# Kernel optimization log

Measured on AMD Instinct MI355X. Metric: run time of the kernel, lower is better.

## Reference

```python
import jax, jax.numpy as jnp
import numpy as np

N = 500_000
E = 16_000_000


def setup_inputs() -> dict:
    key = jax.random.key(0)
    k1, k2, k3, k4, k5 = jax.random.split(key, 5)
    x = jax.random.uniform(k1, (N, 11), dtype=jnp.float32)
    edge_index = jax.random.randint(k2, (2, E), 0, N, dtype=jnp.int32)
    edge_weight = jax.random.uniform(k3, (E,), dtype=jnp.float32)
    W1 = jax.random.normal(k4, (11, 16), dtype=jnp.float32) * 0.3
    b1 = jnp.zeros((16,), jnp.float32)
    W2 = jax.random.normal(k5, (16, 2), dtype=jnp.float32) * 0.3
    b2 = jnp.zeros((2,), jnp.float32)
    return {"x": x, "edge_index": edge_index, "edge_weight": edge_weight,
            "W1": W1, "b1": b1, "W2": W2, "b2": b2}


def gcn_norm(edge_index, edge_weight, n):
    # GCNConv(normalize=True, add_self_loops=True): A_hat = D^-1/2 (A + I) D^-1/2
    self_idx = jnp.arange(n, dtype=edge_index.dtype)
    row = jnp.concatenate([edge_index[0], self_idx])  # source
    col = jnp.concatenate([edge_index[1], self_idx])  # target
    w = jnp.concatenate([edge_weight, jnp.ones((n,), edge_weight.dtype)])
    deg = jax.ops.segment_sum(w, col, num_segments=n)
    dinv = jnp.where(deg > 0, jax.lax.rsqrt(deg), 0.0)
    norm = dinv[row] * w * dinv[col]
    return row, col, norm


def gcn_conv(x, row, col, norm, W, b, n):
    h = x @ W                                   # [N, F_out]
    msg = norm[:, None] * h[row]                # gather + scale, [E+N, F_out]
    out = jax.ops.segment_sum(msg, col, num_segments=n)  # scatter-add
    return out + b


def reference(x, edge_index, edge_weight, W1, b1, W2, b2):
    n = x.shape[0]
    row, col, norm = gcn_norm(edge_index, edge_weight, n)
    h = jax.nn.relu(gcn_conv(x, row, col, norm, W1, b1, n))
    # dropout is identity in eval / deterministic reference
    h = gcn_conv(h, row, col, norm, W2, b2, n)
    return jax.nn.log_softmax(h, axis=1)
```

## Files before the change

kernel.cpp:

```cpp
#include <hip/hip_runtime.h>
#include <math.h>


typedef unsigned long long u64;
typedef unsigned int u32;
typedef unsigned short u16;
typedef _Float16 f16;
typedef __attribute__((ext_vector_type(4))) _Float16 f16x4;

#define BKT    512
#define NBMAX  1024
#define NBLK   512
#define CHUNK  4096


__global__ __launch_bounds__(256) void k_count(const int* __restrict__ col,
                                               u32* __restrict__ hist_g,
                                               int NB, int E, int CH) {
    __shared__ u32 cnt[NBMAX];
    for (int b = threadIdx.x; b < NB; b += 256) cnt[b] = 0;
    __syncthreads();
    int blk = blockIdx.x;
    int s = blk * CH, e = min(s + CH, E);
    for (int i = s + threadIdx.x; i < e; i += 256) {
        int c = __builtin_nontemporal_load(col + i);
        atomicAdd(&cnt[c >> 9], 1u);
    }
    __syncthreads();
    for (int b = threadIdx.x; b < NB; b += 256)
        hist_g[(size_t)blk * NB + b] = cnt[b];
}

__global__ __launch_bounds__(256) void k_colsum(const u32* __restrict__ hist_g,
                                                u32* __restrict__ colsum, int NB) {
    int k = blockIdx.x * 256 + threadIdx.x;
    if (k >= NB) return;
    u32 s = 0;
    for (int j = 0; j < NBLK; j++) s += hist_g[(size_t)j * NB + k];
    colsum[k] = s;
}

__global__ __launch_bounds__(256) void k_scan_sums32(u32* __restrict__ bsum, int nb) {
    __shared__ u32 s[256];
    __shared__ u32 carry;
    int t = threadIdx.x;
    if (t == 0) carry = 0;
    __syncthreads();
    int chunks = (nb + 255) / 256;
    for (int ch = 0; ch < chunks; ch++) {
        int i = ch * 256 + t;
        u32 v = (i < nb) ? bsum[i] : 0;
        s[t] = v;
        __syncthreads();
        for (int off = 1; off < 256; off <<= 1) {
            u32 u = (t >= off) ? s[t - off] : 0;
            __syncthreads();
            s[t] += u;
            __syncthreads();
        }
        u32 incl = s[t];
        u32 my_carry = carry;
        if (i < nb) bsum[i] = incl - v + my_carry;
        __syncthreads();
        if (t == 0) carry = my_carry + s[255];
        __syncthreads();
    }
}

__global__ __launch_bounds__(256) void k_basefill(const u32* __restrict__ hist_g,
                                                  const u32* __restrict__ keybase,
                                                  u32* __restrict__ base_g, int NB) {
    int k = blockIdx.x * 256 + threadIdx.x;
    if (k >= NB) return;
    u32 run = keybase[k];
    for (int j = 0; j < NBLK; j++) {
        base_g[(size_t)j * NB + k] = run;
        run += hist_g[(size_t)j * NB + k];
    }
}


__global__ __launch_bounds__(512) void k_scatter(const int* __restrict__ row,
                                                 const int* __restrict__ col,
                                                 const float* __restrict__ w,
                                                 const u32* __restrict__ base_g,
                                                 u64* __restrict__ edge_g,
                                                 int NB, int E, int CH) {
    __shared__ u64 stage[CHUNK];
    __shared__ u16 skey[CHUNK];
    __shared__ u32 cursor[NBMAX];
    __shared__ u32 ccnt[NBMAX];
    __shared__ u32 cbase[NBMAX];
    __shared__ u32 sscan[512];
    int t = threadIdx.x;
    int blk = blockIdx.x;
    for (int b = t; b < NB; b += 512) cursor[b] = base_g[(size_t)blk * NB + b];
    int s = blk * CH, e = min(s + CH, E);
    for (int c0 = s; c0 < e; c0 += CHUNK) {
        int cend = min(c0 + CHUNK, e);
        for (int b = t; b < NB; b += 512) ccnt[b] = 0;
        __syncthreads();
        u64 rec[8]; u32 rnk[8]; int key[8];
#pragma unroll
        for (int q = 0; q < 8; q++) {
            int i = c0 + q * 512 + t;
            if (i < cend) {
                int c  = __builtin_nontemporal_load(col + i);
                int r  = __builtin_nontemporal_load(row + i);
                float wv = __builtin_nontemporal_load(w + i);
                int k = c >> 9;
                rec[q] = ((u64)__float_as_uint(wv) << 32)
                       | ((u64)(u32)(c & 511) << 19) | (u64)(u32)r;
                key[q] = k;
                rnk[q] = atomicAdd(&ccnt[k], 1u);
            } else key[q] = -1;
        }
        __syncthreads();
        u32 a0 = (2 * t     < NB) ? ccnt[2 * t]     : 0;
        u32 a1 = (2 * t + 1 < NB) ? ccnt[2 * t + 1] : 0;
        sscan[t] = a0 + a1;
        __syncthreads();
        for (int d = 1; d < 512; d <<= 1) {
            u32 v = (t >= d) ? sscan[t - d] : 0;
            __syncthreads();
            sscan[t] += v;
            __syncthreads();
        }
        u32 bse = (t > 0) ? sscan[t - 1] : 0;
        if (2 * t     < NB) cbase[2 * t]     = bse;
        if (2 * t + 1 < NB) cbase[2 * t + 1] = bse + a0;
        __syncthreads();
#pragma unroll
        for (int q = 0; q < 8; q++) {
            if (key[q] >= 0) {
                u32 slot = cbase[key[q]] + rnk[q];
                stage[slot] = rec[q];
                skey[slot] = (u16)key[q];
            }
        }
        __syncthreads();
        int tot = cend - c0;
        for (int j = t; j < tot; j += 512) {
            int k = skey[j];
            edge_g[cursor[k] + (u32)j - cbase[k]] = stage[j];
        }
        __syncthreads();
        for (int b = t; b < NB; b += 512) cursor[b] += ccnt[b];
        __syncthreads();
    }
}


__global__ __launch_bounds__(512) void k_csrsort(const u64* __restrict__ edge_g,
                                                 const u32* __restrict__ kb,
                                                 u64* __restrict__ edge2_g,
                                                 u32* __restrict__ runstart,
                                                 float* __restrict__ dinv_g,
                                                 int NB, int n, int E) {
    __shared__ u64 stage[CHUNK];
    __shared__ u16 skey[CHUNK];
    __shared__ u32 cnt[BKT];
    __shared__ float sdeg[BKT];
    __shared__ u32 cur[BKT];
    __shared__ u32 ccnt[BKT];
    __shared__ u32 cbase[BKT];
    int t = threadIdx.x;
    int b = blockIdx.x;
    int node0 = b << 9;
    int s = (int)kb[b];
    int e = (b + 1 < NB) ? (int)kb[b + 1] : E;
    cnt[t] = 0;
    sdeg[t] = 1.0f;
    __syncthreads();
    for (int i = s + t; i < e; i += 512) {
        u64 rec = __builtin_nontemporal_load(edge_g + i);
        int cl = (int)(((u32)rec >> 19) & 511u);
        atomicAdd(&cnt[cl], 1u);
        atomicAdd(&sdeg[cl], __uint_as_float((u32)(rec >> 32)));
    }
    __syncthreads();
    ccnt[t] = cnt[t];
    __syncthreads();
    for (int d = 1; d < 512; d <<= 1) {
        u32 v = (t >= d) ? ccnt[t - d] : 0;
        __syncthreads();
        ccnt[t] += v;
        __syncthreads();
    }
    u32 mystart = (u32)s + ccnt[t] - cnt[t];
    cur[t] = mystart;
    runstart[node0 + t] = mystart;
    if (t == 511) runstart[node0 + 512] = (u32)e;
    if (node0 + t < n) dinv_g[node0 + t] = rsqrtf(sdeg[t]);
    __syncthreads();
    for (int c0 = s; c0 < e; c0 += CHUNK) {
        int cend = min(c0 + CHUNK, e);
        ccnt[t] = 0;
        __syncthreads();
        u64 rec[8]; u32 rnk[8]; int key[8];
#pragma unroll
        for (int q = 0; q < 8; q++) {
            int i = c0 + q * 512 + t;
            if (i < cend) {
                u64 r = __builtin_nontemporal_load(edge_g + i);
                int cl = (int)(((u32)r >> 19) & 511u);
                rec[q] = r;
                key[q] = cl;
                rnk[q] = atomicAdd(&ccnt[cl], 1u);
            } else key[q] = -1;
        }
        __syncthreads();
        cbase[t] = ccnt[t];
        __syncthreads();
        for (int d = 1; d < 512; d <<= 1) {
            u32 v = (t >= d) ? cbase[t - d] : 0;
            __syncthreads();
            cbase[t] += v;
            __syncthreads();
        }
        u32 myexc = cbase[t] - ccnt[t];
        __syncthreads();
        cbase[t] = myexc;
        __syncthreads();
#pragma unroll
        for (int q = 0; q < 8; q++) {
            if (key[q] >= 0) {
                u32 slot = cbase[key[q]] + rnk[q];
                stage[slot] = rec[q];
                skey[slot] = (u16)key[q];
            }
        }
        __syncthreads();
        int tot = cend - c0;
        for (int j = t; j < tot; j += 512) {
            int k = skey[j];
            edge2_g[cur[k] + (u32)j - cbase[k]] = stage[j];
        }
        __syncthreads();
        cur[t] += ccnt[t];
        __syncthreads();
    }
}


__global__ __launch_bounds__(256) void k_prep(const float* __restrict__ x,
                                              const float* __restrict__ dinv_g,
                                              f16* __restrict__ xs0,
                                              f16* __restrict__ xs1,
                                              f16* __restrict__ xs2, int n) {
    int node = blockIdx.x * 256 + threadIdx.x;
    if (node >= n) return;
    float dv = dinv_g[node];
    const float* xp = x + (size_t)node * 11;
    f16x4 a, bq, c;
#pragma unroll
    for (int k = 0; k < 4; k++) a[k]  = (f16)(dv * xp[k]);
#pragma unroll
    for (int k = 0; k < 4; k++) bq[k] = (f16)(dv * xp[4 + k]);
    c[0] = (f16)(dv * xp[8]);
    c[1] = (f16)(dv * xp[9]);
    c[2] = (f16)(dv * xp[10]);
    c[3] = (f16)0.f;
    *(f16x4*)(xs0 + ((size_t)node << 2)) = a;
    *(f16x4*)(xs1 + ((size_t)node << 2)) = bq;
    *(f16x4*)(xs2 + ((size_t)node << 2)) = c;
}


__global__ __launch_bounds__(256) void k_pass(const u64* __restrict__ edge2_g,
                                              const u32* __restrict__ runstart,
                                              const f16* __restrict__ xsp,
                                              float4* __restrict__ aggp, int n) {
    int node = blockIdx.x * 256 + threadIdx.x;
    if (node >= n) return;
    f16x4 selfv = *(const f16x4*)(xsp + ((size_t)node << 2));
    float a0 = (float)selfv[0], a1 = (float)selfv[1];
    float a2 = (float)selfv[2], a3 = (float)selfv[3];
    int p = (int)runstart[node], pe = (int)runstart[node + 1];
    for (; p + 3 < pe; p += 4) {
        u64 r0 = __builtin_nontemporal_load(edge2_g + p);
        u64 r1 = __builtin_nontemporal_load(edge2_g + p + 1);
        u64 r2 = __builtin_nontemporal_load(edge2_g + p + 2);
        u64 r3 = __builtin_nontemporal_load(edge2_g + p + 3);
        f16x4 g0 = *(const f16x4*)(xsp + ((size_t)((u32)r0 & 0x7FFFFu) << 2));
        f16x4 g1 = *(const f16x4*)(xsp + ((size_t)((u32)r1 & 0x7FFFFu) << 2));
        f16x4 g2 = *(const f16x4*)(xsp + ((size_t)((u32)r2 & 0x7FFFFu) << 2));
        f16x4 g3 = *(const f16x4*)(xsp + ((size_t)((u32)r3 & 0x7FFFFu) << 2));
        float w0 = __uint_as_float((u32)(r0 >> 32));
        float w1 = __uint_as_float((u32)(r1 >> 32));
        float w2 = __uint_as_float((u32)(r2 >> 32));
        float w3 = __uint_as_float((u32)(r3 >> 32));
        a0 += w0 * (float)g0[0] + w1 * (float)g1[0] + w2 * (float)g2[0] + w3 * (float)g3[0];
        a1 += w0 * (float)g0[1] + w1 * (float)g1[1] + w2 * (float)g2[1] + w3 * (float)g3[1];
        a2 += w0 * (float)g0[2] + w1 * (float)g1[2] + w2 * (float)g2[2] + w3 * (float)g3[2];
        a3 += w0 * (float)g0[3] + w1 * (float)g1[3] + w2 * (float)g2[3] + w3 * (float)g3[3];
    }
    for (; p < pe; p++) {
        u64 r0 = edge2_g[p];
        f16x4 g0 = *(const f16x4*)(xsp + ((size_t)((u32)r0 & 0x7FFFFu) << 2));
        float w0 = __uint_as_float((u32)(r0 >> 32));
        a0 += w0 * (float)g0[0];
        a1 += w0 * (float)g0[1];
        a2 += w0 * (float)g0[2];
        a3 += w0 * (float)g0[3];
    }
    float4 ov; ov.x = a0; ov.y = a1; ov.z = a2; ov.w = a3;
    aggp[node] = ov;
}


__global__ __launch_bounds__(256) void k_mlp(const float4* __restrict__ agg0,
                                             const float4* __restrict__ agg1,
                                             const float4* __restrict__ agg2,
                                             const float* __restrict__ dinv_g,
                                             const float* __restrict__ W1,
                                             const float* __restrict__ b1,
                                             const float* __restrict__ W2,
                                             float* __restrict__ h2s, int n) {
    __shared__ float sW1[176];
    __shared__ float sb1[16];
    __shared__ float sW2[32];
    for (int t = threadIdx.x; t < 176; t += 256) sW1[t] = W1[t];
    if (threadIdx.x < 16) sb1[threadIdx.x] = b1[threadIdx.x];
    if (threadIdx.x >= 64 && threadIdx.x < 96) sW2[threadIdx.x - 64] = W2[threadIdx.x - 64];
    __syncthreads();
    int node = blockIdx.x * 256 + threadIdx.x;
    if (node >= n) return;
    float dv = dinv_g[node];
    float4 v0 = agg0[node], v1 = agg1[node], v2 = agg2[node];
    float v[11];
    v[0] = dv * v0.x; v[1] = dv * v0.y; v[2]  = dv * v0.z; v[3] = dv * v0.w;
    v[4] = dv * v1.x; v[5] = dv * v1.y; v[6]  = dv * v1.z; v[7] = dv * v1.w;
    v[8] = dv * v2.x; v[9] = dv * v2.y; v[10] = dv * v2.z;
    float o0 = 0.f, o1 = 0.f;
#pragma unroll
    for (int f = 0; f < 16; f++) {
        float hh = sb1[f];
#pragma unroll
        for (int k = 0; k < 11; k++) hh += v[k] * sW1[k * 16 + f];
        hh = fmaxf(hh, 0.f);
        o0 += hh * sW2[f * 2 + 0];
        o1 += hh * sW2[f * 2 + 1];
    }
    float2 ov; ov.x = dv * o0; ov.y = dv * o1;
    *(float2*)(h2s + ((size_t)node << 1)) = ov;
}


__global__ __launch_bounds__(256) void k_pull2_csr(const u64* __restrict__ edge2_g,
                                                   const u32* __restrict__ runstart,
                                                   const float* __restrict__ h2s,
                                                   const float* __restrict__ dinv_g,
                                                   const float* __restrict__ b2,
                                                   float* __restrict__ out, int n) {
    int node = blockIdx.x * 256 + threadIdx.x;
    if (node >= n) return;
    float2 selfv = *(const float2*)(h2s + (size_t)node * 2);
    float a0 = selfv.x, a1 = selfv.y;
    int p = (int)runstart[node], pe = (int)runstart[node + 1];
    for (; p + 3 < pe; p += 4) {
        u64 r0 = __builtin_nontemporal_load(edge2_g + p);
        u64 r1 = __builtin_nontemporal_load(edge2_g + p + 1);
        u64 r2 = __builtin_nontemporal_load(edge2_g + p + 2);
        u64 r3 = __builtin_nontemporal_load(edge2_g + p + 3);
        float2 g0 = *(const float2*)(h2s + (size_t)((u32)r0 & 0x7FFFFu) * 2);
        float2 g1 = *(const float2*)(h2s + (size_t)((u32)r1 & 0x7FFFFu) * 2);
        float2 g2 = *(const float2*)(h2s + (size_t)((u32)r2 & 0x7FFFFu) * 2);
        float2 g3 = *(const float2*)(h2s + (size_t)((u32)r3 & 0x7FFFFu) * 2);
        float w0 = __uint_as_float((u32)(r0 >> 32));
        float w1 = __uint_as_float((u32)(r1 >> 32));
        float w2 = __uint_as_float((u32)(r2 >> 32));
        float w3 = __uint_as_float((u32)(r3 >> 32));
        a0 += w0 * g0.x + w1 * g1.x + w2 * g2.x + w3 * g3.x;
        a1 += w0 * g0.y + w1 * g1.y + w2 * g2.y + w3 * g3.y;
    }
    for (; p < pe; p++) {
        u64 r0 = edge2_g[p];
        float2 g0 = *(const float2*)(h2s + (size_t)((u32)r0 & 0x7FFFFu) * 2);
        float w0 = __uint_as_float((u32)(r0 >> 32));
        a0 += w0 * g0.x;
        a1 += w0 * g0.y;
    }
    float dv = dinv_g[node];
    float v0 = dv * a0 + b2[0];
    float v1 = dv * a1 + b2[1];
    float m = fmaxf(v0, v1);
    float lse = m + logf(expf(v0 - m) + expf(v1 - m));
    float2 ov; ov.x = v0 - lse; ov.y = v1 - lse;
    *(float2*)(out + (size_t)node * 2) = ov;
}


__global__ __launch_bounds__(256) void k_init_deg(float* deg, int n) {
    int i = blockIdx.x * blockDim.x + threadIdx.x;
    if (i < n) deg[i] = 1.0f;
}

__global__ __launch_bounds__(256) void k_deg_accum(const int* __restrict__ col,
                                                   const float* __restrict__ w,
                                                   float* __restrict__ deg, int E) {
    int i = blockIdx.x * blockDim.x + threadIdx.x;
    if (i < E) atomicAdd(&deg[col[i]], w[i]);
}

__global__ __launch_bounds__(256) void k_rsqrt(float* deg, int n) {
    int i = blockIdx.x * blockDim.x + threadIdx.x;
    if (i < n) {
        float d = deg[i];
        deg[i] = (d > 0.0f) ? rsqrtf(d) : 0.0f;
    }
}

__global__ __launch_bounds__(256) void k_gemm1_plain(const float* __restrict__ x,
                                                     const float* __restrict__ W1,
                                                     float* __restrict__ h1, int n) {
    __shared__ float sW[176];
    for (int t = threadIdx.x; t < 176; t += blockDim.x) sW[t] = W1[t];
    __syncthreads();
    int i = blockIdx.x * blockDim.x + threadIdx.x;
    if (i >= n) return;
    float xi[11];
#pragma unroll
    for (int k = 0; k < 11; k++) xi[k] = x[(size_t)i * 11 + k];
#pragma unroll
    for (int f = 0; f < 16; f++) {
        float acc = 0.0f;
#pragma unroll
        for (int k = 0; k < 11; k++) acc += xi[k] * sW[k * 16 + f];
        h1[(size_t)i * 16 + f] = acc;
    }
}

__global__ __launch_bounds__(256) void k_scatter16(const int* __restrict__ row,
                                                   const int* __restrict__ col,
                                                   const float* __restrict__ w,
                                                   const float* __restrict__ dinv,
                                                   const float* __restrict__ h1,
                                                   float* __restrict__ acc, int E) {
    int i = blockIdx.x * blockDim.x + threadIdx.x;
    if (i >= E) return;
    int r = row[i], c = col[i];
    float nw = dinv[r] * w[i] * dinv[c];
    const float4* hr = (const float4*)(h1 + (size_t)r * 16);
    float* o = acc + (size_t)c * 16;
#pragma unroll
    for (int q = 0; q < 4; q++) {
        float4 hv = hr[q];
        atomicAdd(o + q * 4 + 0, nw * hv.x);
        atomicAdd(o + q * 4 + 1, nw * hv.y);
        atomicAdd(o + q * 4 + 2, nw * hv.z);
        atomicAdd(o + q * 4 + 3, nw * hv.w);
    }
}

__global__ __launch_bounds__(256) void k_post1(const float* __restrict__ h1,
                                               const float* __restrict__ dinv,
                                               const float* __restrict__ b1,
                                               float* __restrict__ acc, int n) {
    int i = blockIdx.x * blockDim.x + threadIdx.x;
    if (i >= n) return;
    float dv = dinv[i];
    float cs = dv * dv;
#pragma unroll
    for (int f = 0; f < 16; f++) {
        float v = acc[(size_t)i * 16 + f] + cs * h1[(size_t)i * 16 + f] + b1[f];
        acc[(size_t)i * 16 + f] = v > 0.0f ? v : 0.0f;
    }
}

__global__ __launch_bounds__(256) void k_gemm2(const float* __restrict__ hrelu,
                                               const float* __restrict__ W2,
                                               float* __restrict__ h2, int n) {
    __shared__ float sW[32];
    for (int t = threadIdx.x; t < 32; t += blockDim.x) sW[t] = W2[t];
    __syncthreads();
    int i = blockIdx.x * blockDim.x + threadIdx.x;
    if (i >= n) return;
    float a0 = 0.0f, a1 = 0.0f;
#pragma unroll
    for (int f = 0; f < 16; f++) {
        float h = hrelu[(size_t)i * 16 + f];
        a0 += h * sW[f * 2 + 0];
        a1 += h * sW[f * 2 + 1];
    }
    h2[(size_t)i * 2 + 0] = a0;
    h2[(size_t)i * 2 + 1] = a1;
}

__global__ __launch_bounds__(256) void k_scatter2(const int* __restrict__ row,
                                                  const int* __restrict__ col,
                                                  const float* __restrict__ w,
                                                  const float* __restrict__ dinv,
                                                  const float* __restrict__ h2,
                                                  float* __restrict__ out, int E) {
    int i = blockIdx.x * blockDim.x + threadIdx.x;
    if (i >= E) return;
    int r = row[i], c = col[i];
    float nw = dinv[r] * w[i] * dinv[c];
    atomicAdd(&out[(size_t)c * 2 + 0], nw * h2[(size_t)r * 2 + 0]);
    atomicAdd(&out[(size_t)c * 2 + 1], nw * h2[(size_t)r * 2 + 1]);
}

__global__ __launch_bounds__(256) void k_final(const float* __restrict__ h2,
                                               const float* __restrict__ dinv,
                                               const float* __restrict__ b2,
                                               float* __restrict__ out, int n) {
    int i = blockIdx.x * blockDim.x + threadIdx.x;
    if (i >= n) return;
    float dv = dinv[i];
    float cs = dv * dv;
    float v0 = out[(size_t)i * 2 + 0] + cs * h2[(size_t)i * 2 + 0] + b2[0];
    float v1 = out[(size_t)i * 2 + 1] + cs * h2[(size_t)i * 2 + 1] + b2[1];
    float m = fmaxf(v0, v1);
    float lse = m + logf(expf(v0 - m) + expf(v1 - m));
    out[(size_t)i * 2 + 0] = v0 - lse;
    out[(size_t)i * 2 + 1] = v1 - lse;
}


static inline size_t align64(size_t x) { return (x + 63) & ~(size_t)63; }

extern "C" void kernel_launch(void* const* d_in, const int* in_sizes, int n_in,
                              void* d_out, int out_size, void* d_ws, size_t ws_size,
                              hipStream_t stream) {
    const float* x  = (const float*)d_in[0];
    const int*   ei = (const int*)d_in[1];
    const float* ew = (const float*)d_in[2];
    const float* W1 = (const float*)d_in[3];
    const float* b1 = (const float*)d_in[4];
    const float* W2 = (const float*)d_in[5];
    const float* b2 = (const float*)d_in[6];

    const int n = in_sizes[0] / 11;
    const int E = in_sizes[2];
    const int* rowp = ei;
    const int* colp = ei + E;

    const int TB = 256;
    const int gN = (n + TB - 1) / TB;
    const int gE = (E + TB - 1) / TB;

    const int NB = (n + BKT - 1) / BKT;
    const int CH = (E + NBLK - 1) / NBLK;

    float* outf = (float*)d_out;

    char* base = (char*)d_ws;
    size_t M = (size_t)NBLK * NB;
    size_t o_hist = 0;
    size_t o_base = align64(o_hist + M * 4);
    size_t o_kb   = align64(o_base + M * 4);
    size_t o_dinv = align64(o_kb + (size_t)(NB + 2) * 4);
    size_t o_xs0  = align64(o_dinv + (size_t)n * 4);
    size_t o_xs1  = align64(o_xs0 + (size_t)n * 8);
    size_t o_xs2  = align64(o_xs1 + (size_t)n * 8);
    size_t o_ag0  = align64(o_xs2 + (size_t)n * 8);
    size_t o_ag1  = align64(o_ag0 + (size_t)n * 16);
    size_t o_ag2  = align64(o_ag1 + (size_t)n * 16);
    size_t o_h2   = align64(o_ag2 + (size_t)n * 16);
    size_t o_run  = align64(o_h2 + (size_t)n * 2 * 4);
    size_t o_edge = align64(o_run + (size_t)(n + BKT + 2) * 4);
    size_t o_edge2 = align64(o_edge + (size_t)E * 8);
    size_t needed = align64(o_edge2 + (size_t)E * 8);

    if (ws_size >= needed && n <= (1 << 19) && NB <= NBMAX) {
        u32*    hist_g = (u32*)(base + o_hist);
        u32*    base_g = (u32*)(base + o_base);
        u32*    kb     = (u32*)(base + o_kb);
        float*  dinv_g = (float*)(base + o_dinv);
        f16*    xs0    = (f16*)(base + o_xs0);
        f16*    xs1    = (f16*)(base + o_xs1);
        f16*    xs2    = (f16*)(base + o_xs2);
        float4* agg0   = (float4*)(base + o_ag0);
        float4* agg1   = (float4*)(base + o_ag1);
        float4* agg2   = (float4*)(base + o_ag2);
        float*  h2s    = (float*)(base + o_h2);
        u32*    runst  = (u32*)(base + o_run);
        u64*    edge_g = (u64*)(base + o_edge);
        u64*    edge2_g = (u64*)(base + o_edge2);

        const int KBg = (NB + 255) / 256;

        k_count<<<NBLK, TB, 0, stream>>>(colp, hist_g, NB, E, CH);
        k_colsum<<<KBg, TB, 0, stream>>>(hist_g, kb, NB);
        k_scan_sums32<<<1, TB, 0, stream>>>(kb, NB);
        k_basefill<<<KBg, TB, 0, stream>>>(hist_g, kb, base_g, NB);
        k_scatter<<<NBLK, 512, 0, stream>>>(rowp, colp, ew, base_g, edge_g, NB, E, CH);
        k_csrsort<<<NB, 512, 0, stream>>>(edge_g, kb, edge2_g, runst, dinv_g, NB, n, E);
        k_prep<<<gN, TB, 0, stream>>>(x, dinv_g, xs0, xs1, xs2, n);
        k_pass<<<gN, TB, 0, stream>>>(edge2_g, runst, xs0, agg0, n);
        k_pass<<<gN, TB, 0, stream>>>(edge2_g, runst, xs1, agg1, n);
        k_pass<<<gN, TB, 0, stream>>>(edge2_g, runst, xs2, agg2, n);
        k_mlp<<<gN, TB, 0, stream>>>(agg0, agg1, agg2, dinv_g, W1, b1, W2, h2s, n);
        k_pull2_csr<<<gN, TB, 0, stream>>>(edge2_g, runst, h2s, dinv_g, b2, outf, n);
    } else {
        float* ws   = (float*)d_ws;
        float* dinv = ws;
        float* h1   = ws + (size_t)n;
        float* acc1 = ws + (size_t)n * 17;

        k_init_deg<<<gN, TB, 0, stream>>>(dinv, n);
        k_deg_accum<<<gE, TB, 0, stream>>>(colp, ew, dinv, E);
        k_rsqrt<<<gN, TB, 0, stream>>>(dinv, n);

        k_gemm1_plain<<<gN, TB, 0, stream>>>(x, W1, h1, n);
        hipMemsetAsync(acc1, 0, (size_t)n * 16 * sizeof(float), stream);
        k_scatter16<<<gE, TB, 0, stream>>>(rowp, colp, ew, dinv, h1, acc1, E);
        k_post1<<<gN, TB, 0, stream>>>(h1, dinv, b1, acc1, n);

        float* h2 = h1;
        k_gemm2<<<gN, TB, 0, stream>>>(acc1, W2, h2, n);
        hipMemsetAsync(outf, 0, (size_t)n * 2 * sizeof(float), stream);
        k_scatter2<<<gE, TB, 0, stream>>>(rowp, colp, ew, dinv, h2, outf, E);
        k_final<<<gN, TB, 0, stream>>>(h2, dinv, b2, outf, n);
    }
}
```

Measured before the change: 1.432 ms.

## Partition layer-1 gather by source-node quarter with full 11-feature rows, fuse MLP

```diff
diff --git a/kernel.cpp b/kernel.cpp
--- a/kernel.cpp
+++ b/kernel.cpp
@@ -6,7 +6,7 @@
 typedef unsigned int u32;
 typedef unsigned short u16;
 typedef _Float16 f16;
-typedef __attribute__((ext_vector_type(4))) _Float16 f16x4;
+typedef __attribute__((ext_vector_type(8))) _Float16 f16x8;
 
 #define BKT    512
 #define NBMAX  1024
@@ -245,105 +245,107 @@
 
 __global__ __launch_bounds__(256) void k_prep(const float* __restrict__ x,
                                               const float* __restrict__ dinv_g,
-                                              f16* __restrict__ xs0,
-                                              f16* __restrict__ xs1,
-                                              f16* __restrict__ xs2, int n) {
+                                              f16* __restrict__ xs, int n) {
     int node = blockIdx.x * 256 + threadIdx.x;
     if (node >= n) return;
     float dv = dinv_g[node];
     const float* xp = x + (size_t)node * 11;
-    f16x4 a, bq, c;
-#pragma unroll
-    for (int k = 0; k < 4; k++) a[k]  = (f16)(dv * xp[k]);
-#pragma unroll
-    for (int k = 0; k < 4; k++) bq[k] = (f16)(dv * xp[4 + k]);
-    c[0] = (f16)(dv * xp[8]);
-    c[1] = (f16)(dv * xp[9]);
-    c[2] = (f16)(dv * xp[10]);
-    c[3] = (f16)0.f;
-    *(f16x4*)(xs0 + ((size_t)node << 2)) = a;
-    *(f16x4*)(xs1 + ((size_t)node << 2)) = bq;
-    *(f16x4*)(xs2 + ((size_t)node << 2)) = c;
+    f16x8 lo, hi;
+#pragma unroll
+    for (int k = 0; k < 8; k++) lo[k] = (f16)(dv * xp[k]);
+    hi[0] = (f16)(dv * xp[8]);
+    hi[1] = (f16)(dv * xp[9]);
+    hi[2] = (f16)(dv * xp[10]);
+    hi[3] = (f16)0.f; hi[4] = (f16)0.f; hi[5] = (f16)0.f;
+    hi[6] = (f16)0.f; hi[7] = (f16)0.f;
+    f16x8* dst = (f16x8*)(xs + ((size_t)node << 4));
+    dst[0] = lo;
+    dst[1] = hi;
 }
 
 
 __global__ __launch_bounds__(256) void k_pass(const u64* __restrict__ edge2_g,
                                               const u32* __restrict__ runstart,
-                                              const f16* __restrict__ xsp,
-                                              float4* __restrict__ aggp, int n) {
-    int node = blockIdx.x * 256 + threadIdx.x;
-    if (node >= n) return;
-    f16x4 selfv = *(const f16x4*)(xsp + ((size_t)node << 2));
-    float a0 = (float)selfv[0], a1 = (float)selfv[1];
-    float a2 = (float)selfv[2], a3 = (float)selfv[3];
-    int p = (int)runstart[node], pe = (int)runstart[node + 1];
-    for (; p + 3 < pe; p += 4) {
-        u64 r0 = __builtin_nontemporal_load(edge2_g + p);
-        u64 r1 = __builtin_nontemporal_load(edge2_g + p + 1);
-        u64 r2 = __builtin_nontemporal_load(edge2_g + p + 2);
-        u64 r3 = __builtin_nontemporal_load(edge2_g + p + 3);
-        f16x4 g0 = *(const f16x4*)(xsp + ((size_t)((u32)r0 & 0x7FFFFu) << 2));
-        f16x4 g1 = *(const f16x4*)(xsp + ((size_t)((u32)r1 & 0x7FFFFu) << 2));
-        f16x4 g2 = *(const f16x4*)(xsp + ((size_t)((u32)r2 & 0x7FFFFu) << 2));
-        f16x4 g3 = *(const f16x4*)(xsp + ((size_t)((u32)r3 & 0x7FFFFu) << 2));
-        float w0 = __uint_as_float((u32)(r0 >> 32));
-        float w1 = __uint_as_float((u32)(r1 >> 32));
-        float w2 = __uint_as_float((u32)(r2 >> 32));
-        float w3 = __uint_as_float((u32)(r3 >> 32));
-        a0 += w0 * (float)g0[0] + w1 * (float)g1[0] + w2 * (float)g2[0] + w3 * (float)g3[0];
-        a1 += w0 * (float)g0[1] + w1 * (float)g1[1] + w2 * (float)g2[1] + w3 * (float)g3[1];
-        a2 += w0 * (float)g0[2] + w1 * (float)g1[2] + w2 * (float)g2[2] + w3 * (float)g3[2];
-        a3 += w0 * (float)g0[3] + w1 * (float)g1[3] + w2 * (float)g2[3] + w3 * (float)g3[3];
-    }
-    for (; p < pe; p++) {
-        u64 r0 = edge2_g[p];
-        f16x4 g0 = *(const f16x4*)(xsp + ((size_t)((u32)r0 & 0x7FFFFu) << 2));
-        float w0 = __uint_as_float((u32)(r0 >> 32));
-        a0 += w0 * (float)g0[0];
-        a1 += w0 * (float)g0[1];
-        a2 += w0 * (float)g0[2];
-        a3 += w0 * (float)g0[3];
-    }
-    float4 ov; ov.x = a0; ov.y = a1; ov.z = a2; ov.w = a3;
-    aggp[node] = ov;
-}
-
-
-__global__ __launch_bounds__(256) void k_mlp(const float4* __restrict__ agg0,
-                                             const float4* __restrict__ agg1,
-                                             const float4* __restrict__ agg2,
-                                             const float* __restrict__ dinv_g,
-                                             const float* __restrict__ W1,
-                                             const float* __restrict__ b1,
-                                             const float* __restrict__ W2,
-                                             float* __restrict__ h2s, int n) {
+                                              const f16* __restrict__ xs,
+                                              float4* __restrict__ agg0,
+                                              float4* __restrict__ agg1,
+                                              float4* __restrict__ agg2,
+                                              const float* __restrict__ dinv_g,
+                                              const float* __restrict__ W1,
+                                              const float* __restrict__ b1,
+                                              const float* __restrict__ W2,
+                                              float* __restrict__ h2s,
+                                              int n, int q, int first, int fin) {
     __shared__ float sW1[176];
     __shared__ float sb1[16];
     __shared__ float sW2[32];
-    for (int t = threadIdx.x; t < 176; t += 256) sW1[t] = W1[t];
-    if (threadIdx.x < 16) sb1[threadIdx.x] = b1[threadIdx.x];
-    if (threadIdx.x >= 64 && threadIdx.x < 96) sW2[threadIdx.x - 64] = W2[threadIdx.x - 64];
-    __syncthreads();
+    if (fin) {
+        for (int t = threadIdx.x; t < 176; t += 256) sW1[t] = W1[t];
+        if (threadIdx.x < 16) sb1[threadIdx.x] = b1[threadIdx.x];
+        if (threadIdx.x >= 32 && threadIdx.x < 64) sW2[threadIdx.x - 32] = W2[threadIdx.x - 32];
+        __syncthreads();
+    }
     int node = blockIdx.x * 256 + threadIdx.x;
     if (node >= n) return;
-    float dv = dinv_g[node];
-    float4 v0 = agg0[node], v1 = agg1[node], v2 = agg2[node];
-    float v[11];
-    v[0] = dv * v0.x; v[1] = dv * v0.y; v[2]  = dv * v0.z; v[3] = dv * v0.w;
-    v[4] = dv * v1.x; v[5] = dv * v1.y; v[6]  = dv * v1.z; v[7] = dv * v1.w;
-    v[8] = dv * v2.x; v[9] = dv * v2.y; v[10] = dv * v2.z;
-    float o0 = 0.f, o1 = 0.f;
-#pragma unroll
-    for (int f = 0; f < 16; f++) {
-        float hh = sb1[f];
-#pragma unroll
-        for (int k = 0; k < 11; k++) hh += v[k] * sW1[k * 16 + f];
-        hh = fmaxf(hh, 0.f);
-        o0 += hh * sW2[f * 2 + 0];
-        o1 += hh * sW2[f * 2 + 1];
-    }
-    float2 ov; ov.x = dv * o0; ov.y = dv * o1;
-    *(float2*)(h2s + ((size_t)node << 1)) = ov;
+    float a[11];
+    if (first) {
+        const f16x8* self = (const f16x8*)(xs + ((size_t)node << 4));
+        f16x8 slo = self[0], shi = self[1];
+#pragma unroll
+        for (int k = 0; k < 8; k++) a[k] = (float)slo[k];
+        a[8] = (float)shi[0]; a[9] = (float)shi[1]; a[10] = (float)shi[2];
+    } else {
+        float4 v0 = agg0[node], v1 = agg1[node], v2 = agg2[node];
+        a[0] = v0.x; a[1] = v0.y; a[2]  = v0.z; a[3] = v0.w;
+        a[4] = v1.x; a[5] = v1.y; a[6]  = v1.z; a[7] = v1.w;
+        a[8] = v2.x; a[9] = v2.y; a[10] = v2.z;
+    }
+    u32 qtag = (u32)q << 17;
+    int p = (int)runstart[node], pe = (int)runstart[node + 1];
+#define PROCQ(rec) { u32 lo_ = (u32)(rec); \
+    if ((lo_ & 0x60000u) == qtag) { \
+        const f16x8* qp_ = (const f16x8*)(xs + ((size_t)(lo_ & 0x7FFFFu) << 4)); \
+        f16x8 l_ = qp_[0], h_ = qp_[1]; \
+        float wv_ = __uint_as_float((u32)((rec) >> 32)); \
+        a[0] += wv_ * (float)l_[0]; a[1] += wv_ * (float)l_[1]; \
+        a[2] += wv_ * (float)l_[2]; a[3] += wv_ * (float)l_[3]; \
+        a[4] += wv_ * (float)l_[4]; a[5] += wv_ * (float)l_[5]; \
+        a[6] += wv_ * (float)l_[6]; a[7] += wv_ * (float)l_[7]; \
+        a[8] += wv_ * (float)h_[0]; a[9] += wv_ * (float)h_[1]; \
+        a[10] += wv_ * (float)h_[2]; } }
+    for (; p + 3 < pe; p += 4) {
+        u64 r0 = edge2_g[p],     r1 = edge2_g[p + 1];
+        u64 r2 = edge2_g[p + 2], r3 = edge2_g[p + 3];
+        PROCQ(r0) PROCQ(r1) PROCQ(r2) PROCQ(r3)
+    }
+    for (; p < pe; p++) {
+        u64 r0 = edge2_g[p];
+        PROCQ(r0)
+    }
+#undef PROCQ
+    if (!fin) {
+        float4 o0, o1, o2;
+        o0.x = a[0]; o0.y = a[1]; o0.z = a[2];  o0.w = a[3];
+        o1.x = a[4]; o1.y = a[5]; o1.z = a[6];  o1.w = a[7];
+        o2.x = a[8]; o2.y = a[9]; o2.z = a[10]; o2.w = 0.f;
+        agg0[node] = o0; agg1[node] = o1; agg2[node] = o2;
+    } else {
+        float dv = dinv_g[node];
+#pragma unroll
+        for (int k = 0; k < 11; k++) a[k] *= dv;
+        float o0 = 0.f, o1 = 0.f;
+#pragma unroll
+        for (int f = 0; f < 16; f++) {
+            float hh = sb1[f];
+#pragma unroll
+            for (int k = 0; k < 11; k++) hh += a[k] * sW1[k * 16 + f];
+            hh = fmaxf(hh, 0.f);
+            o0 += hh * sW2[f * 2 + 0];
+            o1 += hh * sW2[f * 2 + 1];
+        }
+        float2 ov; ov.x = dv * o0; ov.y = dv * o1;
+        *(float2*)(h2s + ((size_t)node << 1)) = ov;
+    }
 }
 
 
@@ -359,10 +361,8 @@
     float a0 = selfv.x, a1 = selfv.y;
     int p = (int)runstart[node], pe = (int)runstart[node + 1];
     for (; p + 3 < pe; p += 4) {
-        u64 r0 = __builtin_nontemporal_load(edge2_g + p);
-        u64 r1 = __builtin_nontemporal_load(edge2_g + p + 1);
-        u64 r2 = __builtin_nontemporal_load(edge2_g + p + 2);
-        u64 r3 = __builtin_nontemporal_load(edge2_g + p + 3);
+        u64 r0 = edge2_g[p],     r1 = edge2_g[p + 1];
+        u64 r2 = edge2_g[p + 2], r3 = edge2_g[p + 3];
         float2 g0 = *(const float2*)(h2s + (size_t)((u32)r0 & 0x7FFFFu) * 2);
         float2 g1 = *(const float2*)(h2s + (size_t)((u32)r1 & 0x7FFFFu) * 2);
         float2 g2 = *(const float2*)(h2s + (size_t)((u32)r2 & 0x7FFFFu) * 2);
@@ -551,10 +551,8 @@
     size_t o_base = align64(o_hist + M * 4);
     size_t o_kb   = align64(o_base + M * 4);
     size_t o_dinv = align64(o_kb + (size_t)(NB + 2) * 4);
-    size_t o_xs0  = align64(o_dinv + (size_t)n * 4);
-    size_t o_xs1  = align64(o_xs0 + (size_t)n * 8);
-    size_t o_xs2  = align64(o_xs1 + (size_t)n * 8);
-    size_t o_ag0  = align64(o_xs2 + (size_t)n * 8);
+    size_t o_xs   = align64(o_dinv + (size_t)n * 4);
+    size_t o_ag0  = align64(o_xs + (size_t)n * 32);
     size_t o_ag1  = align64(o_ag0 + (size_t)n * 16);
     size_t o_ag2  = align64(o_ag1 + (size_t)n * 16);
     size_t o_h2   = align64(o_ag2 + (size_t)n * 16);
@@ -568,9 +566,7 @@
         u32*    base_g = (u32*)(base + o_base);
         u32*    kb     = (u32*)(base + o_kb);
         float*  dinv_g = (float*)(base + o_dinv);
-        f16*    xs0    = (f16*)(base + o_xs0);
-        f16*    xs1    = (f16*)(base + o_xs1);
-        f16*    xs2    = (f16*)(base + o_xs2);
+        f16*    xs     = (f16*)(base + o_xs);
         float4* agg0   = (float4*)(base + o_ag0);
         float4* agg1   = (float4*)(base + o_ag1);
         float4* agg2   = (float4*)(base + o_ag2);
@@ -587,11 +583,15 @@
         k_basefill<<<KBg, TB, 0, stream>>>(hist_g, kb, base_g, NB);
         k_scatter<<<NBLK, 512, 0, stream>>>(rowp, colp, ew, base_g, edge_g, NB, E, CH);
         k_csrsort<<<NB, 512, 0, stream>>>(edge_g, kb, edge2_g, runst, dinv_g, NB, n, E);
-        k_prep<<<gN, TB, 0, stream>>>(x, dinv_g, xs0, xs1, xs2, n);
-        k_pass<<<gN, TB, 0, stream>>>(edge2_g, runst, xs0, agg0, n);
-        k_pass<<<gN, TB, 0, stream>>>(edge2_g, runst, xs1, agg1, n);
-        k_pass<<<gN, TB, 0, stream>>>(edge2_g, runst, xs2, agg2, n);
-        k_mlp<<<gN, TB, 0, stream>>>(agg0, agg1, agg2, dinv_g, W1, b1, W2, h2s, n);
+        k_prep<<<gN, TB, 0, stream>>>(x, dinv_g, xs, n);
+        k_pass<<<gN, TB, 0, stream>>>(edge2_g, runst, xs, agg0, agg1, agg2,
+                                      dinv_g, W1, b1, W2, h2s, n, 0, 1, 0);
+        k_pass<<<gN, TB, 0, stream>>>(edge2_g, runst, xs, agg0, agg1, agg2,
+                                      dinv_g, W1, b1, W2, h2s, n, 1, 0, 0);
+        k_pass<<<gN, TB, 0, stream>>>(edge2_g, runst, xs, agg0, agg1, agg2,
+                                      dinv_g, W1, b1, W2, h2s, n, 2, 0, 0);
+        k_pass<<<gN, TB, 0, stream>>>(edge2_g, runst, xs, agg0, agg1, agg2,
+                                      dinv_g, W1, b1, W2, h2s, n, 3, 0, 1);
         k_pull2_csr<<<gN, TB, 0, stream>>>(edge2_g, runst, h2s, dinv_g, b2, outf, n);
     } else {
         float* ws   = (float*)d_ws;
```

New measurement: 1.367 ms. 1.05x faster.
